# Kernel optimization log

Hardware: AMD Instinct MI355X
Metric: run time of the kernel (lower is better)

## Reference

```python
import jax, jax.numpy as jnp
import numpy as np

B = 8            # batch
I_F = 8192       # infeatures
O_F = 8192       # outfeatures
LUT = 8          # 2**3 lookup entries for 3-bit codes
NNZ_PER_ROW = 128
NUMVALS = O_F * NNZ_PER_ROW


def setup_inputs() -> dict:
    key = jax.random.key(0)
    k0, k1, k2, k3, k4 = jax.random.split(key, 5)
    x = jax.random.normal(k0, (B, I_F), dtype=jnp.float32)
    # 3-bit quantized weight codes, one per (in, out) element
    qidx = jax.random.randint(k1, (I_F, O_F), 0, LUT, dtype=jnp.int32)
    # per-output-channel non-uniform quantization lookup table
    lookup_table = jax.random.normal(k2, (O_F, LUT), dtype=jnp.float32)
    # CSR sparse correction: pack2 inserts NNZ_PER_ROW nonzeros per output row
    rows = jnp.arange(O_F + 1, dtype=jnp.int32) * NNZ_PER_ROW
    cols = jax.random.randint(k3, (NUMVALS,), 0, I_F, dtype=jnp.int32)
    vals = jax.random.normal(k4, (NUMVALS,), dtype=jnp.float32)
    return {"x": x, "qidx": qidx, "lookup_table": lookup_table,
            "rows": rows, "cols": cols, "vals": vals}


def reference(x, qidx, lookup_table, rows, cols, vals):
    # Dequantize: W[i, o] = lookup_table[o, qidx[i, o]]   (per-channel NUQ)
    W = lookup_table[jnp.arange(O_F, dtype=jnp.int32)[None, :], qidx]  # (I, O)
    y = x @ W  # (B, O)
    # CSR sparse correction: row id for each nonzero via searchsorted on rows
    seg = jnp.searchsorted(rows[1:], jnp.arange(NUMVALS, dtype=jnp.int32), side="right")
    contrib = vals[None, :] * x[:, cols]                      # (B, numvals)
    y_sp = jax.ops.segment_sum(contrib.T, seg, num_segments=O_F)  # (O, B)
    return y + y_sp.T
```

## Files before the change

kernel.cpp:

```cpp
#include <hip/hip_runtime.h>

#define I_F 8192
#define O_F 8192
#define NSPLIT 128
#define CHUNK (I_F / NSPLIT)
#define QBATCH 4

__device__ __forceinline__ float lut_sel(const float4& lo, const float4& hi, int q) {
    const bool b2 = (q & 4) != 0;
    const float s0 = b2 ? hi.x : lo.x;
    const float s1 = b2 ? hi.y : lo.y;
    const float s2 = b2 ? hi.z : lo.z;
    const float s3 = b2 ? hi.w : lo.w;
    const bool b1 = (q & 2) != 0;
    const float t0 = b1 ? s2 : s0;
    const float t1 = b1 ? s3 : s1;
    return (q & 1) ? t1 : t0;
}

__global__ __launch_bounds__(256) void prolog_kernel(const float* __restrict__ x,
                                                     float* __restrict__ xT) {
    const int t = blockIdx.x * 256 + threadIdx.x;
    float4 lo, hi;
    lo.x = x[0 * I_F + t];
    lo.y = x[1 * I_F + t];
    lo.z = x[2 * I_F + t];
    lo.w = x[3 * I_F + t];
    hi.x = x[4 * I_F + t];
    hi.y = x[5 * I_F + t];
    hi.z = x[6 * I_F + t];
    hi.w = x[7 * I_F + t];
    ((float4*)xT)[t * 2]     = lo;
    ((float4*)xT)[t * 2 + 1] = hi;
}

__global__ __launch_bounds__(1024, 4) void dense_kernel(const int* __restrict__ qidx,
                                                        const float* __restrict__ lut,
                                                        const float* __restrict__ xT,
                                                        float* __restrict__ P) {
    __shared__ float4 xs[CHUNK][2];

    const int tid = threadIdx.x;
    const int col0 = blockIdx.x * (O_F / 2) + tid * 4;
    const int i0 = blockIdx.y * CHUNK;

    if (tid < CHUNK * 2)
        ((float4*)xs)[tid] = ((const float4*)(xT + (size_t)i0 * 8))[tid];

    float4 lA[4], lB[4];
#pragma unroll
    for (int c = 0; c < 4; ++c) {
        const float4* p = (const float4*)(lut + (size_t)(col0 + c) * 8);
        lA[c] = p[0];
        lB[c] = p[1];
    }

    float acc[4][8];
#pragma unroll
    for (int c = 0; c < 4; ++c)
#pragma unroll
        for (int b = 0; b < 8; ++b) acc[c][b] = 0.0f;

    __syncthreads();

    const int4* qp = (const int4*)(qidx + (size_t)i0 * O_F + col0);

    for (int t = 0; t < CHUNK; t += QBATCH) {
        int4 qb[QBATCH];
#pragma unroll
        for (int k = 0; k < QBATCH; ++k)
            qb[k] = qp[(size_t)(t + k) * (O_F / 4)];

#pragma unroll
        for (int k = 0; k < QBATCH; ++k) {
            const int4   q   = qb[k];
            const float4 xlo = xs[t + k][0];
            const float4 xhi = xs[t + k][1];
#pragma unroll
            for (int c = 0; c < 4; ++c) {
                const int qc = (c == 0) ? q.x : (c == 1) ? q.y : (c == 2) ? q.z : q.w;
                const float w = lut_sel(lA[c], lB[c], qc);
                acc[c][0] += xlo.x * w;
                acc[c][1] += xlo.y * w;
                acc[c][2] += xlo.z * w;
                acc[c][3] += xlo.w * w;
                acc[c][4] += xhi.x * w;
                acc[c][5] += xhi.y * w;
                acc[c][6] += xhi.z * w;
                acc[c][7] += xhi.w * w;
            }
        }
    }

    float* Pb = P + ((size_t)blockIdx.y * 8) * O_F + col0;
#pragma unroll
    for (int b = 0; b < 8; ++b) {
        float4 v = make_float4(acc[0][b], acc[1][b], acc[2][b], acc[3][b]);
        *(float4*)(Pb + (size_t)b * O_F) = v;
    }
}

__global__ __launch_bounds__(256) void sparse_kernel(const int* __restrict__ rows,
                                                     const int* __restrict__ cols,
                                                     const float* __restrict__ vals,
                                                     const float* __restrict__ xT,
                                                     float* __restrict__ sp) {
    const int wave = threadIdx.x >> 6;
    const int lane = threadIdx.x & 63;
    const int o = blockIdx.x * 4 + wave;
    const int r0 = rows[o];
    const int r1 = rows[o + 1];

    float acc[8];
#pragma unroll
    for (int b = 0; b < 8; ++b) acc[b] = 0.0f;

    for (int k = r0 + lane; k < r1; k += 64) {
        const int   col = cols[k];
        const float v   = vals[k];
        const float4* xp = (const float4*)(xT + (size_t)col * 8);
        const float4 xlo = xp[0];
        const float4 xhi = xp[1];
        acc[0] += v * xlo.x;
        acc[1] += v * xlo.y;
        acc[2] += v * xlo.z;
        acc[3] += v * xlo.w;
        acc[4] += v * xhi.x;
        acc[5] += v * xhi.y;
        acc[6] += v * xhi.z;
        acc[7] += v * xhi.w;
    }

#pragma unroll
    for (int s = 1; s < 64; s <<= 1)
#pragma unroll
        for (int b = 0; b < 8; ++b) acc[b] += __shfl_xor(acc[b], s, 64);

    if (lane == 0) {
#pragma unroll
        for (int b = 0; b < 8; ++b) sp[(size_t)b * O_F + o] = acc[b];
    }
}

__global__ __launch_bounds__(64) void reduce_kernel(const float* __restrict__ P,
                                                    const float* __restrict__ sp,
                                                    float* __restrict__ out) {
    const int t4 = blockIdx.x * 64 + threadIdx.x;
    float4 s = ((const float4*)sp)[t4];
#pragma unroll 8
    for (int k = 0; k < NSPLIT; ++k) {
        const float4 p = ((const float4*)P)[(size_t)k * (8 * O_F / 4) + t4];
        s.x += p.x; s.y += p.y; s.z += p.z; s.w += p.w;
    }
    ((float4*)out)[t4] = s;
}

extern "C" void kernel_launch(void* const* d_in, const int* in_sizes, int n_in,
                              void* d_out, int out_size, void* d_ws, size_t ws_size,
                              hipStream_t stream) {
    const float* x    = (const float*)d_in[0];
    const int*   qidx = (const int*)d_in[1];
    const float* lut  = (const float*)d_in[2];
    const int*   rows = (const int*)d_in[3];
    const int*   cols = (const int*)d_in[4];
    const float* vals = (const float*)d_in[5];
    float* out = (float*)d_out;

    float* xT = (float*)d_ws;
    float* sp = xT + (size_t)I_F * 8;
    float* P  = sp + (size_t)O_F * 8;

    prolog_kernel<<<I_F / 256, 256, 0, stream>>>(x, xT);
    dense_kernel<<<dim3(2, NSPLIT), 1024, 0, stream>>>(qidx, lut, xT, P);
    sparse_kernel<<<O_F / 4, 256, 0, stream>>>(rows, cols, vals, xT, sp);
    reduce_kernel<<<(8 * O_F / 4) / 64, 64, 0, stream>>>(P, sp, out);
}
```

Before: 392.0 us.

## Pack 3-bit codes into nibbles in a pre-pass and retile dense kernel

Adds a pack kernel that compresses int32 quantization codes into 4-bit nibbles (8 per word) in a tiled layout, and the dense kernel reads those packed words with 8 columns per thread and 256-thread blocks. The pack pass runs on every call, so it still reads the full 256MB qidx array and also writes a 32MB packed buffer before the dense pass reads it back. The idea trades extra total traffic for a lighter dense kernel with more register reuse per thread.

Result: slower. 436.6 us (+11.4%).

```diff
diff --git a/kernel.cpp b/kernel.cpp
--- a/kernel.cpp
+++ b/kernel.cpp
@@ -3,8 +3,11 @@
 #define I_F 8192
 #define O_F 8192
 #define NSPLIT 128
-#define CHUNK (I_F / NSPLIT)
-#define QBATCH 4
+#define CHUNK 64
+#define NCT 4
+#define CT_COLS 2048
+#define UPR 256
+#define QB 8
 
 __device__ __forceinline__ float lut_sel(const float4& lo, const float4& hi, int q) {
     const bool b2 = (q & 4) != 0;
@@ -34,52 +37,75 @@
     ((float4*)xT)[t * 2 + 1] = hi;
 }
 
-__global__ __launch_bounds__(1024, 4) void dense_kernel(const int* __restrict__ qidx,
-                                                        const float* __restrict__ lut,
-                                                        const float* __restrict__ xT,
-                                                        float* __restrict__ P) {
+__global__ __launch_bounds__(256) void pack_kernel(const int* __restrict__ qidx,
+                                                   unsigned* __restrict__ pk) {
+    const size_t nthr = (size_t)gridDim.x * 256;
+    const size_t total = (size_t)I_F * O_F / 8;
+    for (size_t u = (size_t)blockIdx.x * 256 + threadIdx.x; u < total; u += nthr) {
+        const int4 a = ((const int4*)qidx)[u * 2];
+        const int4 b = ((const int4*)qidx)[u * 2 + 1];
+        const unsigned v = (unsigned)(a.x & 7)        | ((unsigned)(a.y & 7) << 4)  |
+                           ((unsigned)(a.z & 7) << 8) | ((unsigned)(a.w & 7) << 12) |
+                           ((unsigned)(b.x & 7) << 16)| ((unsigned)(b.y & 7) << 20) |
+                           ((unsigned)(b.z & 7) << 24)| ((unsigned)(b.w & 7) << 28);
+        const int row    = (int)(u >> 10);
+        const int colgrp = (int)(u & 1023);
+        const int ct     = colgrp >> 8;
+        const int cg     = colgrp & 255;
+        const int split  = row >> 6;
+        const int r      = row & 63;
+        pk[(((size_t)ct * NSPLIT + split) * CHUNK + r) * UPR + cg] = v;
+    }
+}
+
+__global__ __launch_bounds__(256, 2) void dense_kernel(const unsigned* __restrict__ pk,
+                                                       const float* __restrict__ lut,
+                                                       const float* __restrict__ xT,
+                                                       float* __restrict__ P) {
     __shared__ float4 xs[CHUNK][2];
 
     const int tid = threadIdx.x;
-    const int col0 = blockIdx.x * (O_F / 2) + tid * 4;
-    const int i0 = blockIdx.y * CHUNK;
+    const int ct = blockIdx.x;
+    const int split = blockIdx.y;
+    const int col0 = ct * CT_COLS + tid * 8;
+    const int i0 = split * CHUNK;
 
     if (tid < CHUNK * 2)
         ((float4*)xs)[tid] = ((const float4*)(xT + (size_t)i0 * 8))[tid];
 
-    float4 lA[4], lB[4];
-#pragma unroll
-    for (int c = 0; c < 4; ++c) {
+    float4 lA[8], lB[8];
+#pragma unroll
+    for (int c = 0; c < 8; ++c) {
         const float4* p = (const float4*)(lut + (size_t)(col0 + c) * 8);
         lA[c] = p[0];
         lB[c] = p[1];
     }
 
-    float acc[4][8];
-#pragma unroll
-    for (int c = 0; c < 4; ++c)
+    float acc[8][8];
+#pragma unroll
+    for (int c = 0; c < 8; ++c)
 #pragma unroll
         for (int b = 0; b < 8; ++b) acc[c][b] = 0.0f;
 
     __syncthreads();
 
-    const int4* qp = (const int4*)(qidx + (size_t)i0 * O_F + col0);
-
-    for (int t = 0; t < CHUNK; t += QBATCH) {
-        int4 qb[QBATCH];
-#pragma unroll
-        for (int k = 0; k < QBATCH; ++k)
-            qb[k] = qp[(size_t)(t + k) * (O_F / 4)];
-
-#pragma unroll
-        for (int k = 0; k < QBATCH; ++k) {
-            const int4   q   = qb[k];
+    const unsigned* slab = pk + ((size_t)ct * NSPLIT + split) * (CHUNK * UPR);
+
+    for (int t = 0; t < CHUNK; t += QB) {
+        unsigned qb[QB];
+#pragma unroll
+        for (int k = 0; k < QB; ++k)
+            qb[k] = slab[(t + k) * UPR + tid];
+
+#pragma unroll
+        for (int k = 0; k < QB; ++k) {
+            const unsigned v  = qb[k];
             const float4 xlo = xs[t + k][0];
             const float4 xhi = xs[t + k][1];
 #pragma unroll
-            for (int c = 0; c < 4; ++c) {
-                const int qc = (c == 0) ? q.x : (c == 1) ? q.y : (c == 2) ? q.z : q.w;
-                const float w = lut_sel(lA[c], lB[c], qc);
+            for (int c = 0; c < 8; ++c) {
+                const int q = (int)((v >> (4 * c)) & 7u);
+                const float w = lut_sel(lA[c], lB[c], q);
                 acc[c][0] += xlo.x * w;
                 acc[c][1] += xlo.y * w;
                 acc[c][2] += xlo.z * w;
@@ -92,11 +118,11 @@
         }
     }
 
-    float* Pb = P + ((size_t)blockIdx.y * 8) * O_F + col0;
+    float* Pb = P + ((size_t)split * 8) * O_F + col0;
 #pragma unroll
     for (int b = 0; b < 8; ++b) {
-        float4 v = make_float4(acc[0][b], acc[1][b], acc[2][b], acc[3][b]);
-        *(float4*)(Pb + (size_t)b * O_F) = v;
+        *(float4*)(Pb + (size_t)b * O_F)     = make_float4(acc[0][b], acc[1][b], acc[2][b], acc[3][b]);
+        *(float4*)(Pb + (size_t)b * O_F + 4) = make_float4(acc[4][b], acc[5][b], acc[6][b], acc[7][b]);
     }
 }
 
@@ -169,9 +195,11 @@
     float* xT = (float*)d_ws;
     float* sp = xT + (size_t)I_F * 8;
     float* P  = sp + (size_t)O_F * 8;
+    unsigned* pk = (unsigned*)(P + (size_t)NSPLIT * 8 * O_F);
 
     prolog_kernel<<<I_F / 256, 256, 0, stream>>>(x, xT);
-    dense_kernel<<<dim3(2, NSPLIT), 1024, 0, stream>>>(qidx, lut, xT, P);
+    pack_kernel<<<4096, 256, 0, stream>>>(qidx, pk);
+    dense_kernel<<<dim3(NCT, NSPLIT), 256, 0, stream>>>(pk, lut, xT, P);
     sparse_kernel<<<O_F / 4, 256, 0, stream>>>(rows, cols, vals, xT, sp);
     reduce_kernel<<<(8 * O_F / 4) / 64, 64, 0, stream>>>(P, sp, out);
 }
```
